# Kernel tuning notes

Measured on AMD Instinct MI355X. Metric: run time of the kernel, lower is better.

## Reference

```python
import jax, jax.numpy as jnp
import numpy as np
from jax import lax

# Model dims (match init_kwargs / input_specs)
B, T, N_IN, N_MID, N_OUT = 256, 100, 784, 1024, 10
L_TAU = 0.8  # state decay


def setup_inputs() -> dict:
    key = jax.random.key(0)
    ks = jax.random.split(key, 10)
    x = jax.random.uniform(ks[0], (B, T, N_IN), dtype=jnp.float32)  # input spikes/rates
    y = jax.random.randint(ks[1], (B,), 0, N_OUT, dtype=jnp.int64)

    def lin(k, fan_in, fan_out):
        return jax.random.normal(k, (fan_in, fan_out), dtype=jnp.float32) / np.sqrt(fan_in)

    return {
        "x": x, "y": y,
        "W1": lin(ks[2], N_IN, N_MID),  "b1": jnp.zeros((N_MID,), jnp.float32),
        "W2": lin(ks[3], N_MID, N_MID), "b2": jnp.zeros((N_MID,), jnp.float32),
        "W3": lin(ks[4], N_MID, N_MID), "b3": jnp.zeros((N_MID,), jnp.float32),
        "W4": lin(ks[5], N_MID, N_OUT), "b4": jnp.zeros((N_OUT,), jnp.float32),
    }


def _snu(s, y_prev, x_in, W, b):
    # SNU cell (soft): s_t = relu(W x_t + tau * s_{t-1} * (1 - y_{t-1})); y_t = sigmoid(s_t + b)
    s = jax.nn.relu(x_in @ W + L_TAU * s * (1.0 - y_prev))
    y_out = jax.nn.sigmoid(s + b)
    return s, y_out


def reference(x, y, W1, b1, W2, b2, W3, b3, W4, b4):
    bsz = x.shape[0]
    zeros = lambda n: jnp.zeros((bsz, n), x.dtype)
    carry0 = (zeros(N_MID), zeros(N_MID), zeros(N_MID), zeros(N_MID),
              zeros(N_MID), zeros(N_MID), zeros(N_OUT), zeros(N_OUT))

    def step(carry, x_t):
        s1, y1, s2, y2, s3, y3, s4, y4 = carry
        s1, y1 = _snu(s1, y1, x_t, W1, b1)
        s2, y2 = _snu(s2, y2, y1, W2, b2)
        s3, y3 = _snu(s3, y3, y2, W3, b3)
        s4, y4 = _snu(s4, y4, y3, W4, b4)
        return (s1, y1, s2, y2, s3, y3, s4, y4), y4

    xs = jnp.transpose(x, (1, 0, 2))  # [T, B, n_in]
    _, outs = lax.scan(step, carry0, xs)  # outs: [T, B, n_out]
    # out_rec also stacked the initial zero output; it contributes 0 to the sum
    m = jnp.sum(outs, axis=0)  # [B, n_out]
    logp = jax.nn.log_softmax(m, axis=-1)
    loss = -jnp.mean(jnp.take_along_axis(logp, y[:, None], axis=1))
    return loss, m
```

## Files before the change

### kernel.cpp

```cpp
#include <hip/hip_runtime.h>
#include <hip/hip_bf16.h>


#define BDIM 256
#define TT   100
#define TP   112
#define BB   256
#define MM2  (BB * TP)
#define NMID 1024
#define K1   784
#define K1P  896
#define NOUT 10
#define N4P  16
#define L_TAU 0.8f

typedef __attribute__((ext_vector_type(4))) int   int4x;
typedef __attribute__((ext_vector_type(8))) int   int8x;
typedef __attribute__((ext_vector_type(4))) float f32x4;

__device__ __forceinline__ void async_copy16(const void* g, void* l) {
    __builtin_amdgcn_global_load_lds(
        (const __attribute__((address_space(1))) unsigned int*)g,
        (__attribute__((address_space(3))) unsigned int*)l,
        16, 0, 0);
}

__device__ __forceinline__ unsigned short f2bf(float f) {
    __hip_bfloat16 h = __float2bfloat16(f);
    return __builtin_bit_cast(unsigned short, h);
}
__device__ __forceinline__ float bf2f(unsigned short u) {
    return __uint_as_float((unsigned)u << 16);
}

__global__ void convert_x(const float* __restrict__ X, unsigned char* __restrict__ XB) {
    int m = blockIdx.x;
    int b = m & (BB - 1);
    int t = m >> 8;
    int th = threadIdx.x;
    if (th >= K1P / 4) return;
    int pk = 0;
    if (th < K1 / 4) {
        float4 v = *(const float4*)(X + ((long)b * TT + t) * K1 + th * 4);
        pk = __builtin_amdgcn_cvt_pk_fp8_f32(v.x, v.y, 0, false);
        pk = __builtin_amdgcn_cvt_pk_fp8_f32(v.z, v.w, pk, true);
    }
    *(int*)(XB + ((long)b * TP + t) * K1P + th * 4) = pk;
}

__device__ __forceinline__ void tc_body(const float* __restrict__ W,
                                        unsigned char* __restrict__ WT,
                                        int K, int N, int Kpad,
                                        int bx, int by, int tidx) {
    __shared__ float tile[32][33];
    int k0 = bx * 32;
    int n0 = by * 32;
    int tx = tidx & 31, ty = tidx >> 5;
    #pragma unroll
    for (int i = 0; i < 4; ++i) {
        int k = k0 + ty + i * 8;
        tile[ty + i * 8][tx] = (k < K) ? W[(long)k * N + n0 + tx] : 0.0f;
    }
    __syncthreads();
    int nl = tidx >> 3, kq = tidx & 7;
    int pk = __builtin_amdgcn_cvt_pk_fp8_f32(tile[kq * 4 + 0][nl], tile[kq * 4 + 1][nl], 0, false);
    pk     = __builtin_amdgcn_cvt_pk_fp8_f32(tile[kq * 4 + 2][nl], tile[kq * 4 + 3][nl], pk, true);
    *(int*)(WT + (long)(n0 + nl) * Kpad + k0 + kq * 4) = pk;
}

__global__ void transpose_convert(const float* __restrict__ W, unsigned char* __restrict__ WT,
                                  int K, int N, int Kpad) {
    tc_body(W, WT, K, N, Kpad, blockIdx.x, blockIdx.y, threadIdx.x);
}

__global__ void transpose_convert2(const float* __restrict__ Wa, unsigned char* __restrict__ Ta,
                                   const float* __restrict__ Wb, unsigned char* __restrict__ Tb) {
    const float* W = blockIdx.z ? Wb : Wa;
    unsigned char* T = blockIdx.z ? Tb : Ta;
    tc_body(W, T, NMID, NMID, NMID, blockIdx.x, blockIdx.y, threadIdx.x);
}

__global__ void convert_w4(const float* __restrict__ W4, unsigned char* __restrict__ W4T) {
    int tid = blockIdx.x * BDIM + threadIdx.x;
    int n = tid >> 8;
    int k4 = (tid & 255) * 4;
    float v0 = 0, v1 = 0, v2 = 0, v3 = 0;
    if (n < NOUT) {
        v0 = W4[(k4 + 0) * NOUT + n];
        v1 = W4[(k4 + 1) * NOUT + n];
        v2 = W4[(k4 + 2) * NOUT + n];
        v3 = W4[(k4 + 3) * NOUT + n];
    }
    int pk = __builtin_amdgcn_cvt_pk_fp8_f32(v0, v1, 0, false);
    pk     = __builtin_amdgcn_cvt_pk_fp8_f32(v2, v3, pk, true);
    *(int*)(W4T + (long)n * NMID + k4) = pk;
}

__global__ __launch_bounds__(256) void gemm_snu_fused(
    const unsigned char* __restrict__ A,
    const unsigned char* __restrict__ BT,
    const float* __restrict__ bias,
    unsigned char* __restrict__ Y,
    int Kp)
{
    __shared__ unsigned char smem[30720];
    unsigned char* As = smem;
    unsigned char* Bs = smem + 14336;
    unsigned short* Zs = (unsigned short*)smem;

    const int tid  = threadIdx.x;
    const int wave = tid >> 6;
    const int lane = tid & 63;

    const int l   = blockIdx.x;
    const int xcd = l & 7;
    const int p   = l >> 3;
    const int b   = xcd * 32 + (p >> 3);
    const int bn  = (p & 7) * 128;

    const long arow0 = (long)b * TP;

    f32x4 acc[7][2] = {};

    const int srow = tid >> 3;
    const int lch  = tid & 7;
    const int gch  = lch ^ (srow & 7);
    const unsigned char* Aptr = A  + (arow0 + srow) * Kp + gch * 16;
    const unsigned char* Bptr = BT + (long)(bn + srow) * Kp + gch * 16;

    const int mrow = lane & 15;
    const int g    = lane >> 4;
    const int wc   = wave * 32;

    for (int k0 = 0; k0 < Kp; k0 += 128) {
        #pragma unroll
        for (int i = 0; i < 4; ++i) {
            if (srow + i * 32 < TP)
                async_copy16(Aptr + (long)(i * 32) * Kp + k0,
                             &As[(srow + i * 32) * 128 + lch * 16]);
            async_copy16(Bptr + (long)(i * 32) * Kp + k0,
                         &Bs[(srow + i * 32) * 128 + lch * 16]);
        }
        __syncthreads();

        int8x bfr[2];
        #pragma unroll
        for (int j = 0; j < 2; ++j) {
            int row = wc + j * 16 + mrow;
            int r7  = row & 7;
            int4x lo = *(const int4x*)&Bs[row * 128 + ((2 * g    ) ^ r7) * 16];
            int4x hi = *(const int4x*)&Bs[row * 128 + ((2 * g + 1) ^ r7) * 16];
            bfr[j][0] = lo[0]; bfr[j][1] = lo[1]; bfr[j][2] = lo[2]; bfr[j][3] = lo[3];
            bfr[j][4] = hi[0]; bfr[j][5] = hi[1]; bfr[j][6] = hi[2]; bfr[j][7] = hi[3];
        }
        #pragma unroll
        for (int i = 0; i < 7; ++i) {
            int row = i * 16 + mrow;
            int r7  = row & 7;
            int4x lo = *(const int4x*)&As[row * 128 + ((2 * g    ) ^ r7) * 16];
            int4x hi = *(const int4x*)&As[row * 128 + ((2 * g + 1) ^ r7) * 16];
            int8x af;
            af[0] = lo[0]; af[1] = lo[1]; af[2] = lo[2]; af[3] = lo[3];
            af[4] = hi[0]; af[5] = hi[1]; af[6] = hi[2]; af[7] = hi[3];
            #pragma unroll
            for (int j = 0; j < 2; ++j)
                acc[i][j] = __builtin_amdgcn_mfma_scale_f32_16x16x128_f8f6f4(
                    bfr[j], af, acc[i][j],
                    0, 0,
                    0, 0x7F,
                    0, 0x7F);
        }
        __syncthreads();
    }

    #pragma unroll
    for (int i = 0; i < 7; ++i)
        #pragma unroll
        for (int j = 0; j < 2; ++j) {
            int t  = i * 16 + mrow;
            int nn = wc + j * 16 + g * 4;
            #pragma unroll
            for (int r = 0; r < 4; ++r)
                Zs[(nn + r) * 114 + t] = f2bf(acc[i][j][r]);
        }
    __syncthreads();

    if (tid < 128) {
        int n = tid;
        float bv = bias[bn + n];
        float s = 0.0f, yv = 0.0f;
        const unsigned short* zp = Zs + n * 114;
        unsigned char* yp = Y + arow0 * NMID + bn + n;
        for (int t = 0; t < TT; ++t) {
            float z = bf2f(zp[t]);
            s = fmaxf(fmaf(L_TAU * s, 1.0f - yv, z), 0.0f);
            yv = 1.0f / (1.0f + __expf(-(s + bv)));
            int pk = __builtin_amdgcn_cvt_pk_fp8_f32(yv, yv, 0, false);
            yp[(long)t * NMID] = (unsigned char)(pk & 0xFF);
        }
    }
}

__global__ __launch_bounds__(256) void layer4_gemm(const unsigned char* __restrict__ Y3,
                                                   const unsigned char* __restrict__ W4T,
                                                   float* __restrict__ Z4) {
    const int tid  = threadIdx.x;
    const int wave = tid >> 6;
    const int lane = tid & 63;
    const int mrow = lane & 15;
    const int g    = lane >> 4;
    const int row  = blockIdx.x * 64 + wave * 16 + mrow;
    const unsigned char* ap = Y3  + (long)row  * NMID + g * 32;
    const unsigned char* wp = W4T + (long)mrow * NMID + g * 32;
    f32x4 acc = {};
    #pragma unroll
    for (int kt = 0; kt < 8; ++kt) {
        int4x alo = *(const int4x*)(ap + kt * 128);
        int4x ahi = *(const int4x*)(ap + kt * 128 + 16);
        int4x wlo = *(const int4x*)(wp + kt * 128);
        int4x whi = *(const int4x*)(wp + kt * 128 + 16);
        int8x af, bf;
        af[0] = alo[0]; af[1] = alo[1]; af[2] = alo[2]; af[3] = alo[3];
        af[4] = ahi[0]; af[5] = ahi[1]; af[6] = ahi[2]; af[7] = ahi[3];
        bf[0] = wlo[0]; bf[1] = wlo[1]; bf[2] = wlo[2]; bf[3] = wlo[3];
        bf[4] = whi[0]; bf[5] = whi[1]; bf[6] = whi[2]; bf[7] = whi[3];
        acc = __builtin_amdgcn_mfma_scale_f32_16x16x128_f8f6f4(
            bf, af, acc, 0, 0, 0, 0x7F, 0, 0x7F);
    }
    *(f32x4*)&Z4[(long)row * N4P + g * 4] = acc;
}

__global__ void snu4_recur(const float* __restrict__ Z4, const float* __restrict__ b4,
                           float* __restrict__ m_out) {
    int idx = blockIdx.x * BDIM + threadIdx.x;
    int n = idx & 15;
    int b = idx >> 4;
    if (n >= NOUT) return;
    float bv = b4[n];
    float s = 0.0f, y = 0.0f, msum = 0.0f;
    const float* zp = Z4 + (long)b * TP * N4P + n;
    for (int t0 = 0; t0 < TT; t0 += 4) {
        float z[4];
        #pragma unroll
        for (int j = 0; j < 4; ++j)
            z[j] = zp[(t0 + j) * N4P];
        #pragma unroll
        for (int j = 0; j < 4; ++j) {
            s = fmaxf(fmaf(L_TAU * s, 1.0f - y, z[j]), 0.0f);
            y = 1.0f / (1.0f + __expf(-(s + bv)));
            msum += y;
        }
    }
    m_out[b * NOUT + n] = msum;
}

__global__ void loss_kernel(const float* __restrict__ m, const int* __restrict__ y,
                            float* __restrict__ out) {
    __shared__ float red[BDIM];
    int b = threadIdx.x;
    float v[NOUT];
    float mx = -1e30f;
    #pragma unroll
    for (int n = 0; n < NOUT; ++n) { v[n] = m[b * NOUT + n]; mx = fmaxf(mx, v[n]); }
    float se = 0.0f;
    #pragma unroll
    for (int n = 0; n < NOUT; ++n) se += __expf(v[n] - mx);
    float lse = mx + __logf(se);
    int lbl = y[b];
    float vy = 0.0f;
    #pragma unroll
    for (int n = 0; n < NOUT; ++n) if (n == lbl) vy = v[n];
    red[b] = -(vy - lse);
    __syncthreads();
    for (int off = 128; off; off >>= 1) {
        if (b < off) red[b] += red[b + off];
        __syncthreads();
    }
    if (b == 0) out[0] = red[0] / (float)BB;
}

extern "C" void kernel_launch(void* const* d_in, const int* in_sizes, int n_in,
                              void* d_out, int out_size, void* d_ws, size_t ws_size,
                              hipStream_t stream) {
    const float* x  = (const float*)d_in[0];
    const int*   y  = (const int*)  d_in[1];
    const float* W1 = (const float*)d_in[2];
    const float* b1 = (const float*)d_in[3];
    const float* W2 = (const float*)d_in[4];
    const float* b2 = (const float*)d_in[5];
    const float* W3 = (const float*)d_in[6];
    const float* b3 = (const float*)d_in[7];
    const float* W4 = (const float*)d_in[8];
    const float* b4 = (const float*)d_in[9];
    float* out = (float*)d_out;

    char* ws = (char*)d_ws;
    size_t off = 0;
    auto alloc = [&](size_t bytes) {
        char* p = ws + off;
        off = (off + bytes + 255) & ~(size_t)255;
        return (void*)p;
    };
    unsigned char* XB  = (unsigned char*)alloc((size_t)MM2 * K1P);
    unsigned char* W1T = (unsigned char*)alloc((size_t)NMID * K1P);
    unsigned char* W2T = (unsigned char*)alloc((size_t)NMID * NMID);
    unsigned char* W3T = (unsigned char*)alloc((size_t)NMID * NMID);
    unsigned char* W4T = (unsigned char*)alloc((size_t)N4P * NMID);
    unsigned char* Ya  = (unsigned char*)alloc((size_t)MM2 * NMID);
    unsigned char* Yb  = (unsigned char*)alloc((size_t)MM2 * NMID);
    float*         Z4  = (float*)        alloc((size_t)MM2 * N4P * 4);

    convert_x<<<BB * TT, BDIM, 0, stream>>>(x, XB);
    transpose_convert<<<dim3(K1P / 32, NMID / 32), BDIM, 0, stream>>>(W1, W1T, K1, NMID, K1P);
    transpose_convert2<<<dim3(NMID / 32, NMID / 32, 2), BDIM, 0, stream>>>(W2, W2T, W3, W3T);
    convert_w4<<<N4P * NMID / 4 / BDIM, BDIM, 0, stream>>>(W4, W4T);

    const int fblocks = BB * (NMID / 128);
    gemm_snu_fused<<<fblocks, BDIM, 0, stream>>>(XB, W1T, b1, Ya, K1P);
    gemm_snu_fused<<<fblocks, BDIM, 0, stream>>>(Ya, W2T, b2, Yb, NMID);
    gemm_snu_fused<<<fblocks, BDIM, 0, stream>>>(Yb, W3T, b3, Ya, NMID);
    layer4_gemm<<<MM2 / 64, BDIM, 0, stream>>>(Ya, W4T, Z4);
    snu4_recur<<<(BB * N4P) / BDIM, BDIM, 0, stream>>>(Z4, b4, out + 1);
    loss_kernel<<<1, BDIM, 0, stream>>>(out + 1, y, out);
}
```

Baseline: 357.4 us.

## Double-buffer LDS tiles in fused GEMM and streamline sigmoid recurrence

The fused GEMM+SNU kernel now keeps two LDS buffers and prefetches the next K tile with async global-to-LDS copies while MFMAs run on the current one. This replaces the two per-iteration barriers with a single wait plus barrier. The recurrences in both the fused kernel and snu4_recur now track u = 1 - y through a hardware reciprocal, which shortens the serial dependency chain. The cost is doubled LDS use (about 60KB per block), which may cut occupancy, and the approximate rcp can shift results slightly.

```diff
diff --git a/kernel.cpp b/kernel.cpp
--- a/kernel.cpp
+++ b/kernel.cpp
@@ -14,6 +14,8 @@
 #define N4P  16
 #define L_TAU 0.8f
 
+#define BUFSZ 30720
+
 typedef __attribute__((ext_vector_type(4))) int   int4x;
 typedef __attribute__((ext_vector_type(8))) int   int8x;
 typedef __attribute__((ext_vector_type(4))) float f32x4;
@@ -96,6 +98,20 @@
     *(int*)(W4T + (long)n * NMID + k4) = pk;
 }
 
+__device__ __forceinline__ void stage_tile(const unsigned char* Aptr,
+                                           const unsigned char* Bptr,
+                                           unsigned char* As, unsigned char* Bs,
+                                           int srow, int lch, int Kp, int k0) {
+    #pragma unroll
+    for (int i = 0; i < 4; ++i) {
+        if (srow + i * 32 < TP)
+            async_copy16(Aptr + (long)(i * 32) * Kp + k0,
+                         &As[(srow + i * 32) * 128 + lch * 16]);
+        async_copy16(Bptr + (long)(i * 32) * Kp + k0,
+                     &Bs[(srow + i * 32) * 128 + lch * 16]);
+    }
+}
+
 __global__ __launch_bounds__(256) void gemm_snu_fused(
     const unsigned char* __restrict__ A,
     const unsigned char* __restrict__ BT,
@@ -103,9 +119,7 @@
     unsigned char* __restrict__ Y,
     int Kp)
 {
-    __shared__ unsigned char smem[30720];
-    unsigned char* As = smem;
-    unsigned char* Bs = smem + 14336;
+    __shared__ unsigned char smem[2 * BUFSZ];
     unsigned short* Zs = (unsigned short*)smem;
 
     const int tid  = threadIdx.x;
@@ -132,24 +146,27 @@
     const int g    = lane >> 4;
     const int wc   = wave * 32;
 
+    stage_tile(Aptr, Bptr, smem, smem + 14336, srow, lch, Kp, 0);
+    asm volatile("s_waitcnt vmcnt(0)" ::: "memory");
+    __builtin_amdgcn_s_barrier();
+
+    int cur = 0;
     for (int k0 = 0; k0 < Kp; k0 += 128) {
-        #pragma unroll
-        for (int i = 0; i < 4; ++i) {
-            if (srow + i * 32 < TP)
-                async_copy16(Aptr + (long)(i * 32) * Kp + k0,
-                             &As[(srow + i * 32) * 128 + lch * 16]);
-            async_copy16(Bptr + (long)(i * 32) * Kp + k0,
-                         &Bs[(srow + i * 32) * 128 + lch * 16]);
-        }
-        __syncthreads();
+        unsigned char* Ac = smem + cur;
+        unsigned char* Bc = Ac + 14336;
+
+        if (k0 + 128 < Kp) {
+            unsigned char* An = smem + (cur ^ BUFSZ);
+            stage_tile(Aptr, Bptr, An, An + 14336, srow, lch, Kp, k0 + 128);
+        }
 
         int8x bfr[2];
         #pragma unroll
         for (int j = 0; j < 2; ++j) {
             int row = wc + j * 16 + mrow;
             int r7  = row & 7;
-            int4x lo = *(const int4x*)&Bs[row * 128 + ((2 * g    ) ^ r7) * 16];
-            int4x hi = *(const int4x*)&Bs[row * 128 + ((2 * g + 1) ^ r7) * 16];
+            int4x lo = *(const int4x*)&Bc[row * 128 + ((2 * g    ) ^ r7) * 16];
+            int4x hi = *(const int4x*)&Bc[row * 128 + ((2 * g + 1) ^ r7) * 16];
             bfr[j][0] = lo[0]; bfr[j][1] = lo[1]; bfr[j][2] = lo[2]; bfr[j][3] = lo[3];
             bfr[j][4] = hi[0]; bfr[j][5] = hi[1]; bfr[j][6] = hi[2]; bfr[j][7] = hi[3];
         }
@@ -157,8 +174,8 @@
         for (int i = 0; i < 7; ++i) {
             int row = i * 16 + mrow;
             int r7  = row & 7;
-            int4x lo = *(const int4x*)&As[row * 128 + ((2 * g    ) ^ r7) * 16];
-            int4x hi = *(const int4x*)&As[row * 128 + ((2 * g + 1) ^ r7) * 16];
+            int4x lo = *(const int4x*)&Ac[row * 128 + ((2 * g    ) ^ r7) * 16];
+            int4x hi = *(const int4x*)&Ac[row * 128 + ((2 * g + 1) ^ r7) * 16];
             int8x af;
             af[0] = lo[0]; af[1] = lo[1]; af[2] = lo[2]; af[3] = lo[3];
             af[4] = hi[0]; af[5] = hi[1]; af[6] = hi[2]; af[7] = hi[3];
@@ -170,8 +187,12 @@
                     0, 0x7F,
                     0, 0x7F);
         }
-        __syncthreads();
-    }
+
+        asm volatile("s_waitcnt vmcnt(0)" ::: "memory");
+        __builtin_amdgcn_s_barrier();
+        cur ^= BUFSZ;
+    }
+    __syncthreads();
 
     #pragma unroll
     for (int i = 0; i < 7; ++i)
@@ -188,13 +209,15 @@
     if (tid < 128) {
         int n = tid;
         float bv = bias[bn + n];
-        float s = 0.0f, yv = 0.0f;
+        float s = 0.0f, u = 1.0f;
         const unsigned short* zp = Zs + n * 114;
         unsigned char* yp = Y + arow0 * NMID + bn + n;
         for (int t = 0; t < TT; ++t) {
             float z = bf2f(zp[t]);
-            s = fmaxf(fmaf(L_TAU * s, 1.0f - yv, z), 0.0f);
-            yv = 1.0f / (1.0f + __expf(-(s + bv)));
+            s = fmaxf(fmaf(L_TAU * s, u, z), 0.0f);
+            float e = __expf(s + bv);
+            u = __builtin_amdgcn_rcpf(1.0f + e);
+            float yv = 1.0f - u;
             int pk = __builtin_amdgcn_cvt_pk_fp8_f32(yv, yv, 0, false);
             yp[(long)t * NMID] = (unsigned char)(pk & 0xFF);
         }
@@ -237,7 +260,7 @@
     int b = idx >> 4;
     if (n >= NOUT) return;
     float bv = b4[n];
-    float s = 0.0f, y = 0.0f, msum = 0.0f;
+    float s = 0.0f, u = 1.0f, msum = 0.0f;
     const float* zp = Z4 + (long)b * TP * N4P + n;
     for (int t0 = 0; t0 < TT; t0 += 4) {
         float z[4];
@@ -246,9 +269,10 @@
             z[j] = zp[(t0 + j) * N4P];
         #pragma unroll
         for (int j = 0; j < 4; ++j) {
-            s = fmaxf(fmaf(L_TAU * s, 1.0f - y, z[j]), 0.0f);
-            y = 1.0f / (1.0f + __expf(-(s + bv)));
-            msum += y;
+            s = fmaxf(fmaf(L_TAU * s, u, z[j]), 0.0f);
+            float e = __expf(s + bv);
+            u = __builtin_amdgcn_rcpf(1.0f + e);
+            msum += 1.0f - u;
         }
     }
     m_out[b * NOUT + n] = msum;
```

Result: no change. 360.3 us (+0.8%).

## Widen fused GEMM-SNU tile to 256 columns and use all threads for recurrence

Applied to the files above, without the earlier changes.

The fused GEMM+SNU kernel now covers 256 output columns per block instead of 128. Each wave holds a 7x4 accumulator grid, which halves the number of blocks and the number of times each A row tile is reloaded. All 256 threads now run the serial time recurrence instead of only 128. The sigmoid is rewritten as u = rcp(1+exp(s+b)) with y = 1-u, which avoids a negation and a subtraction on the loop-carried dependency chain. In exchange, registers per thread and LDS per block go up (52 KB), and only 1024 blocks are launched, which may lower occupancy and load balance.

```diff
diff --git a/kernel.cpp b/kernel.cpp
--- a/kernel.cpp
+++ b/kernel.cpp
@@ -14,6 +14,9 @@
 #define N4P  16
 #define L_TAU 0.8f
 
+#define NBLK 256
+#define ZST  102
+
 typedef __attribute__((ext_vector_type(4))) int   int4x;
 typedef __attribute__((ext_vector_type(8))) int   int8x;
 typedef __attribute__((ext_vector_type(4))) float f32x4;
@@ -96,14 +99,29 @@
     *(int*)(W4T + (long)n * NMID + k4) = pk;
 }
 
-__global__ __launch_bounds__(256) void gemm_snu_fused(
+__device__ __forceinline__ void stage_tile(const unsigned char* Aptr,
+                                           const unsigned char* Bptr,
+                                           unsigned char* As, unsigned char* Bs,
+                                           int srow, int lch, int Kp, int k0) {
+    #pragma unroll
+    for (int i = 0; i < 4; ++i)
+        if (srow + i * 32 < TP)
+            async_copy16(Aptr + (long)(i * 32) * Kp + k0,
+                         &As[(srow + i * 32) * 128 + lch * 16]);
+    #pragma unroll
+    for (int i = 0; i < 8; ++i)
+        async_copy16(Bptr + (long)(i * 32) * Kp + k0,
+                     &Bs[(srow + i * 32) * 128 + lch * 16]);
+}
+
+__global__ __launch_bounds__(256, 3) void gemm_snu_fused(
     const unsigned char* __restrict__ A,
     const unsigned char* __restrict__ BT,
     const float* __restrict__ bias,
     unsigned char* __restrict__ Y,
     int Kp)
 {
-    __shared__ unsigned char smem[30720];
+    __shared__ unsigned char smem[52224];
     unsigned char* As = smem;
     unsigned char* Bs = smem + 14336;
     unsigned short* Zs = (unsigned short*)smem;
@@ -115,12 +133,12 @@
     const int l   = blockIdx.x;
     const int xcd = l & 7;
     const int p   = l >> 3;
-    const int b   = xcd * 32 + (p >> 3);
-    const int bn  = (p & 7) * 128;
+    const int b   = xcd * 32 + (p >> 2);
+    const int bn  = (p & 3) * NBLK;
 
     const long arow0 = (long)b * TP;
 
-    f32x4 acc[7][2] = {};
+    f32x4 acc[7][4] = {};
 
     const int srow = tid >> 3;
     const int lch  = tid & 7;
@@ -130,22 +148,15 @@
 
     const int mrow = lane & 15;
     const int g    = lane >> 4;
-    const int wc   = wave * 32;
+    const int wc   = wave * 64;
 
     for (int k0 = 0; k0 < Kp; k0 += 128) {
-        #pragma unroll
-        for (int i = 0; i < 4; ++i) {
-            if (srow + i * 32 < TP)
-                async_copy16(Aptr + (long)(i * 32) * Kp + k0,
-                             &As[(srow + i * 32) * 128 + lch * 16]);
-            async_copy16(Bptr + (long)(i * 32) * Kp + k0,
-                         &Bs[(srow + i * 32) * 128 + lch * 16]);
-        }
+        stage_tile(Aptr, Bptr, As, Bs, srow, lch, Kp, k0);
         __syncthreads();
 
-        int8x bfr[2];
-        #pragma unroll
-        for (int j = 0; j < 2; ++j) {
+        int8x bfr[4];
+        #pragma unroll
+        for (int j = 0; j < 4; ++j) {
             int row = wc + j * 16 + mrow;
             int r7  = row & 7;
             int4x lo = *(const int4x*)&Bs[row * 128 + ((2 * g    ) ^ r7) * 16];
@@ -163,7 +174,7 @@
             af[0] = lo[0]; af[1] = lo[1]; af[2] = lo[2]; af[3] = lo[3];
             af[4] = hi[0]; af[5] = hi[1]; af[6] = hi[2]; af[7] = hi[3];
             #pragma unroll
-            for (int j = 0; j < 2; ++j)
+            for (int j = 0; j < 4; ++j)
                 acc[i][j] = __builtin_amdgcn_mfma_scale_f32_16x16x128_f8f6f4(
                     bfr[j], af, acc[i][j],
                     0, 0,
@@ -176,25 +187,28 @@
     #pragma unroll
     for (int i = 0; i < 7; ++i)
         #pragma unroll
-        for (int j = 0; j < 2; ++j) {
+        for (int j = 0; j < 4; ++j) {
             int t  = i * 16 + mrow;
             int nn = wc + j * 16 + g * 4;
-            #pragma unroll
-            for (int r = 0; r < 4; ++r)
-                Zs[(nn + r) * 114 + t] = f2bf(acc[i][j][r]);
+            if (t < TT)
+                #pragma unroll
+                for (int r = 0; r < 4; ++r)
+                    Zs[(nn + r) * ZST + t] = f2bf(acc[i][j][r]);
         }
     __syncthreads();
 
-    if (tid < 128) {
+    {
         int n = tid;
         float bv = bias[bn + n];
-        float s = 0.0f, yv = 0.0f;
-        const unsigned short* zp = Zs + n * 114;
+        float s = 0.0f, u = 1.0f;
+        const unsigned short* zp = Zs + n * ZST;
         unsigned char* yp = Y + arow0 * NMID + bn + n;
         for (int t = 0; t < TT; ++t) {
             float z = bf2f(zp[t]);
-            s = fmaxf(fmaf(L_TAU * s, 1.0f - yv, z), 0.0f);
-            yv = 1.0f / (1.0f + __expf(-(s + bv)));
+            s = fmaxf(fmaf(L_TAU * s, u, z), 0.0f);
+            float e = __expf(s + bv);
+            u = __builtin_amdgcn_rcpf(1.0f + e);
+            float yv = 1.0f - u;
             int pk = __builtin_amdgcn_cvt_pk_fp8_f32(yv, yv, 0, false);
             yp[(long)t * NMID] = (unsigned char)(pk & 0xFF);
         }
@@ -237,7 +251,7 @@
     int b = idx >> 4;
     if (n >= NOUT) return;
     float bv = b4[n];
-    float s = 0.0f, y = 0.0f, msum = 0.0f;
+    float s = 0.0f, u = 1.0f, msum = 0.0f;
     const float* zp = Z4 + (long)b * TP * N4P + n;
     for (int t0 = 0; t0 < TT; t0 += 4) {
         float z[4];
@@ -246,9 +260,10 @@
             z[j] = zp[(t0 + j) * N4P];
         #pragma unroll
         for (int j = 0; j < 4; ++j) {
-            s = fmaxf(fmaf(L_TAU * s, 1.0f - y, z[j]), 0.0f);
-            y = 1.0f / (1.0f + __expf(-(s + bv)));
-            msum += y;
+            s = fmaxf(fmaf(L_TAU * s, u, z[j]), 0.0f);
+            float e = __expf(s + bv);
+            u = __builtin_amdgcn_rcpf(1.0f + e);
+            msum += 1.0f - u;
         }
     }
     m_out[b * NOUT + n] = msum;
@@ -315,7 +330,7 @@
     transpose_convert2<<<dim3(NMID / 32, NMID / 32, 2), BDIM, 0, stream>>>(W2, W2T, W3, W3T);
     convert_w4<<<N4P * NMID / 4 / BDIM, BDIM, 0, stream>>>(W4, W4T);
 
-    const int fblocks = BB * (NMID / 128);
+    const int fblocks = BB * (NMID / NBLK);
     gemm_snu_fused<<<fblocks, BDIM, 0, stream>>>(XB, W1T, b1, Ya, K1P);
     gemm_snu_fused<<<fblocks, BDIM, 0, stream>>>(Ya, W2T, b2, Yb, NMID);
     gemm_snu_fused<<<fblocks, BDIM, 0, stream>>>(Yb, W3T, b3, Ya, NMID);
```

Result: faster. 336.7 us (-5.8%).
